# Kernel tuning notes

Hardware: AMD Instinct MI355X
Metric: run time of the kernel (lower is better)

The kernel has to match this reference:

```python
import jax, jax.numpy as jnp
from jax import lax
import numpy as np

N, C, H, W = 16, 128, 128, 128
CH = C // 4  # adapter contraction channels


def setup_inputs() -> dict:
    key = jax.random.key(0)
    ks = jax.random.split(key, 12)
    x = jax.random.normal(ks[0], (N, C, H, W), jnp.float32)
    # intensity in {1,2,3} as the torch module expects (intensity[i]-1 indexes adapters)
    intensity = jax.random.randint(ks[1], (N,), 1, 4)
    conv1_w = jax.random.normal(ks[2], (C, C, 3, 3), jnp.float32) * 0.02
    conv1_b = jnp.zeros((C,), jnp.float32)
    prelu1 = jnp.float32(0.25)  # nn.PReLU default single shared slope
    conv2_w = jax.random.normal(ks[3], (C, C, 3, 3), jnp.float32) * 0.02
    conv2_b = jnp.zeros((C,), jnp.float32)
    # 3 adapter experts, stacked on leading axis
    aW1 = jax.random.normal(ks[4], (3, CH, C), jnp.float32) * 0.05
    ab1 = jnp.zeros((3, CH), jnp.float32)
    aW2 = jax.random.normal(ks[5], (3, C, CH), jnp.float32) * 0.05
    ab2 = jnp.zeros((3, C), jnp.float32)
    prelu2 = jnp.float32(0.25)
    return dict(x=x, intensity=intensity, conv1_w=conv1_w, conv1_b=conv1_b,
                prelu1=prelu1, conv2_w=conv2_w, conv2_b=conv2_b,
                aW1=aW1, ab1=ab1, aW2=aW2, ab2=ab2, prelu2=prelu2)


def prelu(x, a):
    return jnp.where(x >= 0, x, a * x)


def conv3x3(x, w, b):
    y = lax.conv_general_dilated(x, w, window_strides=(1, 1),
                                 padding=((1, 1), (1, 1)),
                                 dimension_numbers=('NCHW', 'OIHW', 'NCHW'))
    return y + b[None, :, None, None]


def reference(x, intensity, conv1_w, conv1_b, prelu1, conv2_w, conv2_b,
              aW1, ab1, aW2, ab2, prelu2):
    h = prelu(conv3x3(x, conv1_w, conv1_b), prelu1)      # conv1 + PReLU
    h = conv3x3(h, conv2_w, conv2_b)                     # conv2, no activation
    x1 = jnp.mean(h, axis=(2, 3))                        # AdaptiveAvgPool2d(1)+Flatten -> [N,C]
    idx = intensity - 1                                  # expert id per sample
    W1, b1 = aW1[idx], ab1[idx]                          # gather per-sample expert weights
    W2, b2 = aW2[idx], ab2[idx]
    a = jax.nn.relu(jnp.einsum('nc,nhc->nh', x1, W1) + b1)
    g = jnp.einsum('nh,nch->nc', a, W2) + b2             # [N,C]
    out = h * jax.nn.sigmoid(g)[:, :, None, None] + x    # gated residual
    return prelu(out, prelu2)
```

## Files before the change

kernel.cpp:

```cpp
#include <hip/hip_runtime.h>
#include <hip/hip_bf16.h>
#include <math.h>

#define NN   16
#define C_   128
#define HH   128
#define WW   128
#define CHID 32
#define NTILES 64

#define BCHUNK 33792

typedef short bf16x8 __attribute__((ext_vector_type(8)));
typedef float f32x4  __attribute__((ext_vector_type(4)));

__device__ inline void glds16(const void* g, void* l) {
    __builtin_amdgcn_global_load_lds(
        (const __attribute__((address_space(1))) unsigned int*)g,
        (__attribute__((address_space(3))) unsigned int*)l, 16, 0, 0);
}

__device__ inline unsigned short f2bf(float f) {
    __hip_bfloat16 h = __float2bfloat16(f);
    return *reinterpret_cast<unsigned short*>(&h);
}

__global__ __launch_bounds__(64) void pack_w_k(
    const float* __restrict__ w1, const float* __restrict__ w2,
    unsigned short* __restrict__ wl)
{
    const int b = blockIdx.x;
    const int conv = b / 288, rem = b % 288;
    const int kk = rem / 32, ck = (rem % 32) / 8, cot = rem % 8;
    const int l = threadIdx.x;
    const int co  = cot * 16 + (l & 15);
    const int ci0 = ck * 32 + (l >> 4) * 8;
    const float* W = conv ? w2 : w1;
    union { unsigned short u[8]; uint4 v; } pk;
#pragma unroll
    for (int j = 0; j < 8; ++j)
        pk.u[j] = f2bf(W[(size_t)(co * C_ + ci0 + j) * 9 + kk]);
    unsigned short* dst = wl + (size_t)conv * 147456 +
        ((((size_t)kk * 4 + ck) * 8 + cot) * 64 + l) * 8;
    *reinterpret_cast<uint4*>(dst) = pk.v;
}

__global__ __launch_bounds__(256) void to_cnhwc_k(
    const float* __restrict__ x, unsigned short* __restrict__ xb)
{
    __shared__ unsigned short s_t[128][136];
    const int y = blockIdx.x, n = blockIdx.y, t = threadIdx.x;

#pragma unroll
    for (int p = 0; p < 16; ++p) {
        int fi = p * 256 + t;
        int ci = fi >> 5, x0 = (fi & 31) * 4;
        float4 v = *reinterpret_cast<const float4*>(
            x + (((size_t)(n * C_ + ci) * HH) + y) * WW + x0);
        const int slot = ((ci >> 3) ^ ((x0 >> 2) & 7)) * 8 + (ci & 7);
        s_t[x0 + 0][slot] = f2bf(v.x);
        s_t[x0 + 1][slot] = f2bf(v.y);
        s_t[x0 + 2][slot] = f2bf(v.z);
        s_t[x0 + 3][slot] = f2bf(v.w);
    }
    __syncthreads();
    unsigned short* dstbase = xb + ((size_t)(n * HH + y)) * 16384;
#pragma unroll
    for (int p = 0; p < 8; ++p) {
        int o = p * 256 + t;
        int ck = o >> 9, u = o & 511;
        int xc = u >> 2, q = u & 3;
        int k = ck * 4 + q;
        uint4 v = *reinterpret_cast<const uint4*>(
            &s_t[xc][(k ^ ((xc >> 2) & 7)) * 8]);
        *reinterpret_cast<uint4*>(dstbase + (size_t)ck * 4096 + xc * 32 + q * 8) = v;
    }
}

template<int CONV>
__global__ __launch_bounds__(512) void conv_mfma_k(
    const unsigned short* __restrict__ inb,
    const unsigned short* __restrict__ wl,
    const float* __restrict__ bias,
    const float* __restrict__ prelu_a,
    unsigned short* __restrict__ outb,
    float* __restrict__ outf,
    float* __restrict__ partial)
{
    __shared__ char  smem[2 * BCHUNK];
    __shared__ float s_part[8][64];

    const int tid = threadIdx.x;
    const int l = tid & 63, w = tid >> 6;
    const int wco = w >> 2, wy = (w >> 1) & 1, wxh = w & 1;
    const int lg = l >> 4, l15 = l & 15;
    const int yp = blockIdx.x, n = blockIdx.z;
    const int y0 = yp * 2;

    const f32x4 fz = {0.f, 0.f, 0.f, 0.f};
    f32x4 acc[4][4];
#pragma unroll
    for (int m = 0; m < 4; ++m)
#pragma unroll
        for (int nf = 0; nf < 4; ++nf) acc[m][nf] = fz;

    const bf16x8* wv = reinterpret_cast<const bf16x8*>(wl);
    const uint4 z4 = {0u, 0u, 0u, 0u};

    auto stage = [&](int ck, char* sb) {
        const int r = w >> 1, xh = w & 1;
        const int ygl = y0 - 1 + r;
        if (ygl < 0 || ygl >= HH) {
            int t2 = xh * 64 + l;
            for (int i = t2; i < 528; i += 128)
                *reinterpret_cast<uint4*>(sb + r * 8448 + i * 16) = z4;
        } else {
            if (xh == 0 && l < 8) {
                int col = (l < 4) ? 0 : 129, q = l & 3;
                *reinterpret_cast<uint4*>(sb + r * 8448 + col * 64 + q * 16) = z4;
            }
            size_t rowbase = (((size_t)(n * HH + ygl)) * 4 + ck) * 8192;
#pragma unroll
            for (int i = 0; i < 4; ++i) {
                const int p  = xh * 64 + i * 16 + (l >> 2);
                const int sd = (l & 3) ^ (((1 + p) >> 1) & 3);
                const char* g = (const char*)inb + rowbase + (size_t)p * 64 + sd * 16;
                glds16(g, sb + r * 8448 + (1 + xh * 64 + i * 16) * 64);
            }
        }
    };

    stage(0, smem);
    __syncthreads();

    for (int ck = 0; ck < 4; ++ck) {
        char* sb = smem + (ck & 1) * BCHUNK;
        if (ck < 3) stage(ck + 1, smem + ((ck + 1) & 1) * BCHUNK);

        bf16x8 a_cur[4];
#pragma unroll
        for (int m = 0; m < 4; ++m)
            a_cur[m] = wv[(((size_t)0 * 4 + ck) * 8 + wco * 4 + m) * 64 + l];

#pragma unroll
        for (int kk = 0; kk < 9; ++kk) {
            const int ky = kk / 3, kx = kk % 3;
            bf16x8 a_nxt[4];
            if (kk < 8) {
#pragma unroll
                for (int m = 0; m < 4; ++m)
                    a_nxt[m] = wv[((((size_t)kk + 1) * 4 + ck) * 8 + wco * 4 + m) * 64 + l];
            }
            const int rrow = wy + ky;
            bf16x8 b[4];
#pragma unroll
            for (int nf = 0; nf < 4; ++nf) {
                int xi = wxh * 64 + nf * 16 + l15 + kx;
                int slot = lg ^ ((xi >> 1) & 3);
                b[nf] = *reinterpret_cast<const bf16x8*>(
                    sb + rrow * 8448 + xi * 64 + slot * 16);
            }
#pragma unroll
            for (int nf = 0; nf < 4; ++nf)
#pragma unroll
                for (int m = 0; m < 4; ++m)
                    acc[m][nf] = __builtin_amdgcn_mfma_f32_16x16x32_bf16(
                        a_cur[m], b[nf], acc[m][nf], 0, 0, 0);
            if (kk < 8) {
#pragma unroll
                for (int m = 0; m < 4; ++m) a_cur[m] = a_nxt[m];
            }
        }
        __syncthreads();
    }

    const int ybase = y0 + wy;
    if (CONV == 1) {
        const float a1 = *prelu_a;
        unsigned short (*s_rp)[136] = reinterpret_cast<unsigned short (*)[136]>(smem);
        for (int r = 0; r < 2; ++r) {
            if (wy == r) {
#pragma unroll
                for (int m = 0; m < 4; ++m) {
                    const int co0 = wco * 64 + m * 16 + lg * 4;
#pragma unroll
                    for (int nf = 0; nf < 4; ++nf) {
                        const int xc = wxh * 64 + nf * 16 + l15;
                        union { unsigned short u[4]; uint2 v; } pk;
#pragma unroll
                        for (int jj = 0; jj < 4; ++jj) {
                            float f = acc[m][nf][jj] + bias[co0 + jj];
                            f = (f >= 0.f) ? f : a1 * f;
                            pk.u[jj] = f2bf(f);
                        }
                        *reinterpret_cast<uint2*>(&s_rp[xc][co0]) = pk.v;
                    }
                }
            }
            __syncthreads();
            const int y = y0 + r;
#pragma unroll
            for (int p = 0; p < 4; ++p) {
                int u = p * 512 + tid;
                int xc = u >> 4, k = u & 15;
                uint4 v = *reinterpret_cast<const uint4*>(&s_rp[xc][k * 8]);
                *reinterpret_cast<uint4*>(outb +
                    (((size_t)(n * HH + y)) * 4 + (k >> 2)) * 4096 +
                    xc * 32 + (k & 3) * 8) = v;
            }
            __syncthreads();
        }
    } else {
        float ps[4][4];
#pragma unroll
        for (int m = 0; m < 4; ++m)
#pragma unroll
            for (int jj = 0; jj < 4; ++jj) ps[m][jj] = 0.f;
#pragma unroll
        for (int m = 0; m < 4; ++m) {
            const int co0 = wco * 64 + m * 16 + lg * 4;
#pragma unroll
            for (int nf = 0; nf < 4; ++nf) {
                const int xc = wxh * 64 + nf * 16 + l15;
#pragma unroll
                for (int jj = 0; jj < 4; ++jj) {
                    float f = acc[m][nf][jj] + bias[co0 + jj];
                    outf[(((size_t)(n * C_ + co0 + jj)) * HH + ybase) * WW + xc] = f;
                    ps[m][jj] += f;
                }
            }
        }
#pragma unroll
        for (int m = 0; m < 4; ++m)
#pragma unroll
            for (int jj = 0; jj < 4; ++jj) {
                float s = ps[m][jj];
                s += __shfl_xor(s, 1); s += __shfl_xor(s, 2);
                s += __shfl_xor(s, 4); s += __shfl_xor(s, 8);
                ps[m][jj] = s;
            }
        if (l15 == 0) {
#pragma unroll
            for (int m = 0; m < 4; ++m)
#pragma unroll
                for (int jj = 0; jj < 4; ++jj)
                    s_part[w][m * 16 + lg * 4 + jj] = ps[m][jj];
        }
        __syncthreads();
        if (tid < C_) {
            const int half = tid >> 6;
            float s = 0.f;
#pragma unroll
            for (int w2 = 0; w2 < 4; ++w2) s += s_part[half * 4 + w2][tid & 63];
            partial[((size_t)(n * C_ + tid)) * NTILES + yp] = s;
        }
    }
}

__global__ __launch_bounds__(C_) void adapter_k(
    const float* __restrict__ partial, const int* __restrict__ intensity,
    const float* __restrict__ aW1, const float* __restrict__ ab1,
    const float* __restrict__ aW2, const float* __restrict__ ab2,
    float* __restrict__ sig)
{
    __shared__ float sx[C_];
    __shared__ float sa[CHID];
    const int n = blockIdx.x, c = threadIdx.x;

    float s = 0.f;
    for (int t = 0; t < NTILES; ++t)
        s += partial[(size_t)(n * C_ + c) * NTILES + t];
    sx[c] = s * (1.f / (float)(HH * WW));
    __syncthreads();

    const int idx = intensity[n] - 1;
    if (c < CHID) {
        float a = ab1[idx * CHID + c];
        const float* wrow = aW1 + (size_t)(idx * CHID + c) * C_;
        for (int k = 0; k < C_; ++k) a = fmaf(wrow[k], sx[k], a);
        sa[c] = fmaxf(a, 0.f);
    }
    __syncthreads();

    float g = ab2[idx * C_ + c];
    const float* w2row = aW2 + (size_t)(idx * C_ + c) * CHID;
#pragma unroll
    for (int k = 0; k < CHID; ++k) g = fmaf(w2row[k], sa[k], g);
    sig[n * C_ + c] = 1.f / (1.f + expf(-g));
}

__global__ __launch_bounds__(256) void epilogue_k(
    const float* __restrict__ x, const float* __restrict__ sig,
    const float* __restrict__ prelu_a, float* __restrict__ out, int total4)
{
    const float a = *prelu_a;
    const int stride = gridDim.x * blockDim.x;
    for (int i = blockIdx.x * blockDim.x + threadIdx.x; i < total4; i += stride) {
        const int nc = (i * 4) >> 14;
        const float s = sig[nc];
        float4 h4 = ((const float4*)out)[i];
        float4 x4 = ((const float4*)x)[i];
        float4 v;
        v.x = h4.x * s + x4.x;  v.x = (v.x >= 0.f) ? v.x : a * v.x;
        v.y = h4.y * s + x4.y;  v.y = (v.y >= 0.f) ? v.y : a * v.y;
        v.z = h4.z * s + x4.z;  v.z = (v.z >= 0.f) ? v.z : a * v.z;
        v.w = h4.w * s + x4.w;  v.w = (v.w >= 0.f) ? v.w : a * v.w;
        ((float4*)out)[i] = v;
    }
}

extern "C" void kernel_launch(void* const* d_in, const int* in_sizes, int n_in,
                              void* d_out, int out_size, void* d_ws, size_t ws_size,
                              hipStream_t stream)
{
    const float* x         = (const float*)d_in[0];
    const int*   intensity = (const int*)  d_in[1];
    const float* w1        = (const float*)d_in[2];
    const float* b1        = (const float*)d_in[3];
    const float* p1        = (const float*)d_in[4];
    const float* w2        = (const float*)d_in[5];
    const float* b2        = (const float*)d_in[6];
    const float* aW1       = (const float*)d_in[7];
    const float* ab1       = (const float*)d_in[8];
    const float* aW2       = (const float*)d_in[9];
    const float* ab2       = (const float*)d_in[10];
    const float* p2        = (const float*)d_in[11];
    float* out = (float*)d_out;

    unsigned short* xb = (unsigned short*)d_out;

    unsigned short* h1b = (unsigned short*)d_ws;
    unsigned short* wl  = (unsigned short*)((char*)d_ws + (size_t)33554432 * 2);
    float* partial = (float*)((char*)wl + (size_t)294912 * 2);
    float* sig     = partial + (size_t)NN * C_ * NTILES;

    pack_w_k<<<dim3(576), dim3(64), 0, stream>>>(w1, w2, wl);
    to_cnhwc_k<<<dim3(HH, NN), dim3(256), 0, stream>>>(x, xb);

    conv_mfma_k<1><<<dim3(NTILES, 1, NN), dim3(512), 0, stream>>>(
        xb, wl, b1, p1, h1b, nullptr, nullptr);
    conv_mfma_k<2><<<dim3(NTILES, 1, NN), dim3(512), 0, stream>>>(
        h1b, wl + (size_t)147456, b2, nullptr, nullptr, out, partial);

    adapter_k<<<dim3(NN), dim3(C_), 0, stream>>>(
        partial, intensity, aW1, ab1, aW2, ab2, sig);

    const int total4 = NN * C_ * HH * WW / 4;
    epilogue_k<<<dim3(2048), dim3(256), 0, stream>>>(x, sig, p2, out, total4);
}
```

Baseline: 309.1 us.

## Store conv2 output as bf16 and fuse transpose into residual epilogue

Conv2 now writes its output as bf16 in the channel-blocked layout when the workspace is large enough, and a new per-row epilogue kernel transposes it through shared memory while applying the gate, residual and PReLU. This avoids writing the fp32 conv2 result and reading it back. The activation layout changes from 32-channel to 16-channel slabs, and the conv drops double buffering for a single LDS buffer, using an input-chunk rotation per block to spread memory traffic. Rounding the conv2 output to bf16 before the residual adds precision loss, and losing the prefetch overlap may slow the conv loop.

Measured after the change: 262.0 us. 1.18x faster.

```diff
diff --git a/kernel.cpp b/kernel.cpp
--- a/kernel.cpp
+++ b/kernel.cpp
@@ -8,8 +8,6 @@
 #define WW   128
 #define CHID 32
 #define NTILES 64
-
-#define BCHUNK 33792
 
 typedef short bf16x8 __attribute__((ext_vector_type(8)));
 typedef float f32x4  __attribute__((ext_vector_type(4)));
@@ -68,16 +66,16 @@
 #pragma unroll
     for (int p = 0; p < 8; ++p) {
         int o = p * 256 + t;
-        int ck = o >> 9, u = o & 511;
-        int xc = u >> 2, q = u & 3;
-        int k = ck * 4 + q;
+        int sl = o >> 8, u = o & 255;
+        int xc = u >> 1, q = u & 1;
+        int oct = sl * 2 + q;
         uint4 v = *reinterpret_cast<const uint4*>(
-            &s_t[xc][(k ^ ((xc >> 2) & 7)) * 8]);
-        *reinterpret_cast<uint4*>(dstbase + (size_t)ck * 4096 + xc * 32 + q * 8) = v;
-    }
-}
-
-template<int CONV>
+            &s_t[xc][(oct ^ ((xc >> 2) & 7)) * 8]);
+        *reinterpret_cast<uint4*>(dstbase + (size_t)sl * 2048 + xc * 16 + q * 8) = v;
+    }
+}
+
+template<int MODE>
 __global__ __launch_bounds__(512) void conv_mfma_k(
     const unsigned short* __restrict__ inb,
     const unsigned short* __restrict__ wl,
@@ -87,7 +85,7 @@
     float* __restrict__ outf,
     float* __restrict__ partial)
 {
-    __shared__ char  smem[2 * BCHUNK];
+    __shared__ char  smem[34816];
     __shared__ float s_part[8][64];
 
     const int tid = threadIdx.x;
@@ -96,6 +94,7 @@
     const int lg = l >> 4, l15 = l & 15;
     const int yp = blockIdx.x, n = blockIdx.z;
     const int y0 = yp * 2;
+    const int rot = (yp + n) & 3;
 
     const f32x4 fz = {0.f, 0.f, 0.f, 0.f};
     f32x4 acc[4][4];
@@ -105,9 +104,10 @@
         for (int nf = 0; nf < 4; ++nf) acc[m][nf] = fz;
 
     const bf16x8* wv = reinterpret_cast<const bf16x8*>(wl);
+    char* sb = smem;
     const uint4 z4 = {0u, 0u, 0u, 0u};
 
-    auto stage = [&](int ck, char* sb) {
+    auto stage = [&](int ck) {
         const int r = w >> 1, xh = w & 1;
         const int ygl = y0 - 1 + r;
         if (ygl < 0 || ygl >= HH) {
@@ -119,23 +119,23 @@
                 int col = (l < 4) ? 0 : 129, q = l & 3;
                 *reinterpret_cast<uint4*>(sb + r * 8448 + col * 64 + q * 16) = z4;
             }
-            size_t rowbase = (((size_t)(n * HH + ygl)) * 4 + ck) * 8192;
+            const size_t rowbase = ((size_t)(n * HH + ygl)) * 32768;
 #pragma unroll
             for (int i = 0; i < 4; ++i) {
                 const int p  = xh * 64 + i * 16 + (l >> 2);
                 const int sd = (l & 3) ^ (((1 + p) >> 1) & 3);
-                const char* g = (const char*)inb + rowbase + (size_t)p * 64 + sd * 16;
+                const char* g = (const char*)inb + rowbase +
+                    (size_t)(2 * ck + (sd >> 1)) * 4096 + p * 32 + (sd & 1) * 16;
                 glds16(g, sb + r * 8448 + (1 + xh * 64 + i * 16) * 64);
             }
         }
     };
 
-    stage(0, smem);
-    __syncthreads();
-
-    for (int ck = 0; ck < 4; ++ck) {
-        char* sb = smem + (ck & 1) * BCHUNK;
-        if (ck < 3) stage(ck + 1, smem + ((ck + 1) & 1) * BCHUNK);
+    for (int c8 = 0; c8 < 4; ++c8) {
+        const int ck = (c8 + rot) & 3;
+        __syncthreads();
+        stage(ck);
+        __syncthreads();
 
         bf16x8 a_cur[4];
 #pragma unroll
@@ -171,12 +171,19 @@
                 for (int m = 0; m < 4; ++m) a_cur[m] = a_nxt[m];
             }
         }
-        __syncthreads();
-    }
+    }
+    __syncthreads();
 
     const int ybase = y0 + wy;
-    if (CONV == 1) {
-        const float a1 = *prelu_a;
+    if (MODE == 0 || MODE == 1) {
+        const float a1 = (MODE == 0) ? *prelu_a : 0.f;
+        float ps[4][4];
+        if (MODE == 1) {
+#pragma unroll
+            for (int m = 0; m < 4; ++m)
+#pragma unroll
+                for (int jj = 0; jj < 4; ++jj) ps[m][jj] = 0.f;
+        }
         unsigned short (*s_rp)[136] = reinterpret_cast<unsigned short (*)[136]>(smem);
         for (int r = 0; r < 2; ++r) {
             if (wy == r) {
@@ -190,7 +197,8 @@
 #pragma unroll
                         for (int jj = 0; jj < 4; ++jj) {
                             float f = acc[m][nf][jj] + bias[co0 + jj];
-                            f = (f >= 0.f) ? f : a1 * f;
+                            if (MODE == 0) f = (f >= 0.f) ? f : a1 * f;
+                            else           ps[m][jj] += f;
                             pk.u[jj] = f2bf(f);
                         }
                         *reinterpret_cast<uint2*>(&s_rp[xc][co0]) = pk.v;
@@ -205,10 +213,36 @@
                 int xc = u >> 4, k = u & 15;
                 uint4 v = *reinterpret_cast<const uint4*>(&s_rp[xc][k * 8]);
                 *reinterpret_cast<uint4*>(outb +
-                    (((size_t)(n * HH + y)) * 4 + (k >> 2)) * 4096 +
-                    xc * 32 + (k & 3) * 8) = v;
+                    (((size_t)(n * HH + y)) * 8 + (k >> 1)) * 2048 +
+                    xc * 16 + (k & 1) * 8) = v;
             }
             __syncthreads();
+        }
+        if (MODE == 1) {
+#pragma unroll
+            for (int m = 0; m < 4; ++m)
+#pragma unroll
+                for (int jj = 0; jj < 4; ++jj) {
+                    float s = ps[m][jj];
+                    s += __shfl_xor(s, 1); s += __shfl_xor(s, 2);
+                    s += __shfl_xor(s, 4); s += __shfl_xor(s, 8);
+                    ps[m][jj] = s;
+                }
+            if (l15 == 0) {
+#pragma unroll
+                for (int m = 0; m < 4; ++m)
+#pragma unroll
+                    for (int jj = 0; jj < 4; ++jj)
+                        s_part[w][m * 16 + lg * 4 + jj] = ps[m][jj];
+            }
+            __syncthreads();
+            if (tid < C_) {
+                const int half = tid >> 6;
+                float s = 0.f;
+#pragma unroll
+                for (int w2 = 0; w2 < 4; ++w2) s += s_part[half * 4 + w2][tid & 63];
+                partial[((size_t)(n * C_ + tid)) * NTILES + yp] = s;
+            }
         }
     } else {
         float ps[4][4];
@@ -287,6 +321,53 @@
 #pragma unroll
     for (int k = 0; k < CHID; ++k) g = fmaf(w2row[k], sa[k], g);
     sig[n * C_ + c] = 1.f / (1.f + expf(-g));
+}
+
+__global__ __launch_bounds__(256) void epilogue_bf16_k(
+    const unsigned short* __restrict__ h2b, const float* __restrict__ x,
+    const float* __restrict__ sig, const float* __restrict__ prelu_a,
+    float* __restrict__ out)
+{
+    __shared__ unsigned short s_h[128][136];
+    const int y = blockIdx.x, n = blockIdx.y, t = threadIdx.x;
+    const float a = *prelu_a;
+    const unsigned short* slab = h2b + ((size_t)(n * HH + y)) * 16384;
+
+#pragma unroll
+    for (int p = 0; p < 8; ++p) {
+        int o = p * 256 + t;
+        int sl = o >> 8, u = o & 255;
+        int xc = u >> 1, q = u & 1;
+        int oct = sl * 2 + q;
+        uint4 v = *reinterpret_cast<const uint4*>(
+            slab + (size_t)sl * 2048 + xc * 16 + q * 8);
+        *reinterpret_cast<uint4*>(&s_h[xc][(oct ^ ((xc >> 2) & 7)) * 8]) = v;
+    }
+    __syncthreads();
+
+#pragma unroll
+    for (int p = 0; p < 16; ++p) {
+        int fi = p * 256 + t;
+        int ci = fi >> 5, x0 = (fi & 31) * 4;
+        const float sg = sig[n * C_ + ci];
+        float4 x4 = *reinterpret_cast<const float4*>(
+            x + (((size_t)(n * C_ + ci)) * HH + y) * WW + x0);
+        float4 v;
+        float hv[4];
+#pragma unroll
+        for (int j = 0; j < 4; ++j) {
+            int xr = x0 + j;
+            unsigned short hu = s_h[xr][((ci >> 3) ^ ((xr >> 2) & 7)) * 8 + (ci & 7)];
+            unsigned int bits = ((unsigned int)hu) << 16;
+            hv[j] = *reinterpret_cast<float*>(&bits);
+        }
+        v.x = hv[0] * sg + x4.x;  v.x = (v.x >= 0.f) ? v.x : a * v.x;
+        v.y = hv[1] * sg + x4.y;  v.y = (v.y >= 0.f) ? v.y : a * v.y;
+        v.z = hv[2] * sg + x4.z;  v.z = (v.z >= 0.f) ? v.z : a * v.z;
+        v.w = hv[3] * sg + x4.w;  v.w = (v.w >= 0.f) ? v.w : a * v.w;
+        *reinterpret_cast<float4*>(
+            out + (((size_t)(n * C_ + ci)) * HH + y) * WW + x0) = v;
+    }
 }
 
 __global__ __launch_bounds__(256) void epilogue_k(
@@ -327,24 +408,45 @@
     const float* p2        = (const float*)d_in[11];
     float* out = (float*)d_out;
 
-    unsigned short* xb = (unsigned short*)d_out;
+    const size_t SLAB = (size_t)33554432 * 2;
+    const size_t WLB  = (size_t)294912 * 2;
+    const size_t NEED = 2 * SLAB + WLB + (size_t)(NN * C_ * NTILES + NN * C_ + 64) * 4;
+    const bool big = ws_size >= NEED;
 
     unsigned short* h1b = (unsigned short*)d_ws;
-    unsigned short* wl  = (unsigned short*)((char*)d_ws + (size_t)33554432 * 2);
-    float* partial = (float*)((char*)wl + (size_t)294912 * 2);
+    unsigned short* xb;
+    unsigned short* h2b = nullptr;
+    unsigned short* wl;
+    if (big) {
+        xb  = (unsigned short*)((char*)d_ws + SLAB);
+        h2b = xb;
+        wl  = (unsigned short*)((char*)d_ws + 2 * SLAB);
+    } else {
+        xb  = (unsigned short*)d_out;
+        wl  = (unsigned short*)((char*)d_ws + SLAB);
+    }
+    float* partial = (float*)((char*)wl + WLB);
     float* sig     = partial + (size_t)NN * C_ * NTILES;
 
     pack_w_k<<<dim3(576), dim3(64), 0, stream>>>(w1, w2, wl);
     to_cnhwc_k<<<dim3(HH, NN), dim3(256), 0, stream>>>(x, xb);
 
-    conv_mfma_k<1><<<dim3(NTILES, 1, NN), dim3(512), 0, stream>>>(
+    conv_mfma_k<0><<<dim3(NTILES, 1, NN), dim3(512), 0, stream>>>(
         xb, wl, b1, p1, h1b, nullptr, nullptr);
-    conv_mfma_k<2><<<dim3(NTILES, 1, NN), dim3(512), 0, stream>>>(
-        h1b, wl + (size_t)147456, b2, nullptr, nullptr, out, partial);
-
-    adapter_k<<<dim3(NN), dim3(C_), 0, stream>>>(
-        partial, intensity, aW1, ab1, aW2, ab2, sig);
-
-    const int total4 = NN * C_ * HH * WW / 4;
-    epilogue_k<<<dim3(2048), dim3(256), 0, stream>>>(x, sig, p2, out, total4);
-}
+
+    if (big) {
+        conv_mfma_k<1><<<dim3(NTILES, 1, NN), dim3(512), 0, stream>>>(
+            h1b, wl + (size_t)147456, b2, nullptr, h2b, nullptr, partial);
+        adapter_k<<<dim3(NN), dim3(C_), 0, stream>>>(
+            partial, intensity, aW1, ab1, aW2, ab2, sig);
+        epilogue_bf16_k<<<dim3(HH, NN), dim3(256), 0, stream>>>(
+            h2b, x, sig, p2, out);
+    } else {
+        conv_mfma_k<2><<<dim3(NTILES, 1, NN), dim3(512), 0, stream>>>(
+            h1b, wl + (size_t)147456, b2, nullptr, nullptr, out, partial);
+        adapter_k<<<dim3(NN), dim3(C_), 0, stream>>>(
+            partial, intensity, aW1, ab1, aW2, ab2, sig);
+        const int total4 = NN * C_ * HH * WW / 4;
+        epilogue_k<<<dim3(2048), dim3(256), 0, stream>>>(x, sig, p2, out, total4);
+    }
+}
```
